# Kernel optimization log

Hardware: AMD Instinct MI355X
Metric: run time of the kernel (lower is better)

The kernel has to match this reference:

```python
import jax, jax.numpy as jnp
import numpy as np

EPS = 1e-5  # torch LayerNorm default

def _ln(x, g, b):
    m = jnp.mean(x, axis=-1, keepdims=True)
    v = jnp.mean((x - m) ** 2, axis=-1, keepdims=True)
    return (x - m) * jax.lax.rsqrt(v + EPS) * g + b

def setup_inputs() -> dict:
    key = jax.random.key(0)
    ks = jax.random.split(key, 12)
    N_sup = N_res = 768
    c_z = 128   # input_dim
    c = 128     # num_intermediate_channel
    c_out = 128 # output_dim
    s = 0.02
    d = {}
    d["act_s"] = jax.random.normal(ks[0], (N_sup, N_sup, c_z), jnp.float32)
    d["act_r"] = jax.random.normal(ks[1], (N_res, N_res, c_z), jnp.float32)
    d["mask_r"] = (jax.random.uniform(ks[2], (N_res, N_res)) > 0.1).astype(jnp.float32)
    # input LayerNorm params
    d["ln_in_g"] = jnp.ones((c_z,), jnp.float32)
    d["ln_in_b"] = jnp.zeros((c_z,), jnp.float32)
    # projections (stored as [in, out], y = x @ W + b)
    d["w_lp"] = (jax.random.normal(ks[3], (c_z, c)) * s).astype(jnp.float32)
    d["b_lp"] = jnp.zeros((c,), jnp.float32)
    d["w_rp"] = (jax.random.normal(ks[4], (c_z, c)) * s).astype(jnp.float32)
    d["b_rp"] = jnp.zeros((c,), jnp.float32)
    # gates (bias_init=1)
    d["w_lg"] = (jax.random.normal(ks[5], (c_z, c)) * s).astype(jnp.float32)
    d["b_lg"] = jnp.ones((c,), jnp.float32)
    d["w_rg"] = (jax.random.normal(ks[6], (c_z, c)) * s).astype(jnp.float32)
    d["b_rg"] = jnp.ones((c,), jnp.float32)
    # center LayerNorm
    d["ln_c_g"] = jnp.ones((c,), jnp.float32)
    d["ln_c_b"] = jnp.zeros((c,), jnp.float32)
    # output projection
    d["w_out"] = (jax.random.normal(ks[7], (c, c_out)) * s).astype(jnp.float32)
    d["b_out"] = jnp.zeros((c_out,), jnp.float32)
    return d

def reference(act_s, act_r, mask_r, ln_in_g, ln_in_b, w_lp, b_lp, w_rp, b_rp,
              w_lg, b_lg, w_rg, b_rg, ln_c_g, ln_c_b, w_out, b_out):
    m = mask_r[..., None]                                   # [N_res, N_res, 1]
    s = _ln(act_s, ln_in_g, ln_in_b)                        # [N_sup, N_sup, c_z]
    r = _ln(act_r, ln_in_g, ln_in_b)                        # [N_res, N_res, c_z]
    left = (s @ w_lp + b_lp) * jax.nn.sigmoid(s @ w_lg + b_lg)
    right = (m * (r @ w_rp + b_rp)) * jax.nn.sigmoid(r @ w_rg + b_rg)
    left_line = left.sum(axis=0)                            # [N_sup, c] (aggr_by_row)
    right_line = right.sum(axis=0)                          # [N_res, c]
    act = jnp.einsum('ik,jk->ijk', left_line, right_line)   # [N_sup, N_res, c]
    act = _ln(act, ln_c_g, ln_c_b)
    return act @ w_out + b_out                              # [N_sup, N_res, c_out]
```

## Files before the change

kernel.cpp:

```cpp
#include <hip/hip_runtime.h>
#include <math.h>

#define NRES 768
#define C    128
#define LNEPS 1e-5f
#define TA   16
#define ACH  48
#define MI   16
#define NIT  (NRES / MI)
#define XBUF (MI * 256)
#define LHALF (ACH * NIT)

typedef __attribute__((ext_vector_type(8))) short bf16x8;
typedef __attribute__((ext_vector_type(4))) float f32x4;

__device__ __forceinline__ uint32_t pack_hi(uint32_t u0, uint32_t u1) {
    return (u1 & 0xFFFF0000u) | (u0 >> 16);
}

__device__ __forceinline__ void split2t(float a, float b, uint32_t& hi, uint32_t& lo) {
    const uint32_t ua = __float_as_uint(a), ub = __float_as_uint(b);
    const float ra = a - __uint_as_float(ua & 0xFFFF0000u);
    const float rb = b - __uint_as_float(ub & 0xFFFF0000u);
    hi = pack_hi(ua, ub);
    lo = pack_hi(__float_as_uint(ra), __float_as_uint(rb));
}

__device__ __forceinline__ void stage_row3(const float4& x, int row, int t,
                                           char* hiB, char* loB, char* sqB) {
    const int byte = (row * 256 + 8 * (t & 31)) ^ ((row & 15) << 4);
    uint2 uh, ul, uq;
    split2t(x.x, x.y, uh.x, ul.x);
    split2t(x.z, x.w, uh.y, ul.y);
    uq.x = pack_hi(__float_as_uint(x.x * x.x), __float_as_uint(x.y * x.y));
    uq.y = pack_hi(__float_as_uint(x.z * x.z), __float_as_uint(x.w * x.w));
    *(uint2*)(hiB + byte) = uh;
    *(uint2*)(loB + byte) = ul;
    *(uint2*)(sqB + byte) = uq;
}

__device__ __forceinline__ uint32_t bf16rn(float f) {
    uint32_t u = __float_as_uint(f);
    return (u + 0x7FFFu + ((u >> 16) & 1u)) >> 16;
}

__global__ __launch_bounds__(256, 3) void line_all(
    const float* __restrict__ act_s, const float* __restrict__ act_r,
    const float* __restrict__ mask,
    const float* __restrict__ ln_g, const float* __restrict__ ln_b,
    const float* __restrict__ w_lp, const float* __restrict__ b_lp,
    const float* __restrict__ w_rp, const float* __restrict__ b_rp,
    const float* __restrict__ w_lg, const float* __restrict__ b_lg,
    const float* __restrict__ w_rg, const float* __restrict__ b_rg,
    float* __restrict__ part)
{
    __shared__ char  sHi[XBUF];
    __shared__ char  sLo[XBUF];
    __shared__ char  sSq[XBUF];
    __shared__ float sM[TA * MI];

    const int t = threadIdx.x;
    const int w = t >> 6;
    const int l = t & 63;
    const int right = (blockIdx.x >= LHALF);
    const int bid2  = blockIdx.x - right * LHALF;
    const int i0  = (bid2 % NIT) * MI;
    const int ach = bid2 / NIT;
    const int a0  = ach * TA;

    const float* act = right ? act_r : act_s;
    const float* wP  = right ? w_rp : w_lp;
    const float* bP  = right ? b_rp : b_lp;
    const float* wG  = right ? w_rg : w_lg;
    const float* bG  = right ? b_rg : b_lg;

    bf16x8 bfr[4][4];
    float  sQ[4], cB[4];
#pragma unroll
    for (int nt = 0; nt < 4; ++nt) {
        const float* wsrc = (nt < 2) ? wP : wG;
        const int n = w * 32 + (nt & 1) * 16 + (l & 15);
        float sacc = 0.f, tacc = 0.f;
#pragma unroll
        for (int kk = 0; kk < 4; ++kk) {
            bf16x8 f;
#pragma unroll
            for (int jj = 0; jj < 8; ++jj) {
                const int k = kk * 32 + (l >> 4) * 8 + jj;
                const float wv = wsrc[k * C + n];
                const uint32_t q = bf16rn(ln_g[k] * wv);
                f[jj] = (short)q;
                sacc += __uint_as_float(q << 16);
                tacc += ln_b[k] * wv;
            }
            bfr[nt][kk] = f;
        }
        sacc += __shfl_xor(sacc, 16); sacc += __shfl_xor(sacc, 32);
        tacc += __shfl_xor(tacc, 16); tacc += __shfl_xor(tacc, 32);
        sQ[nt] = sacc;
        cB[nt] = tacc + ((nt < 2) ? bP[n] : bG[n]);
    }

    bf16x8 onesf;
#pragma unroll
    for (int jj = 0; jj < 8; ++jj) onesf[jj] = (short)0x3F80;

    if (right) {
        sM[t] = mask[(size_t)(a0 + (t >> 4)) * NRES + i0 + (t & 15)];
    }

    float lacc[2][4];
#pragma unroll
    for (int ntp = 0; ntp < 2; ++ntp)
#pragma unroll
        for (int jr = 0; jr < 4; ++jr) lacc[ntp][jr] = 0.f;

    const float* srcbase = act + (size_t)a0 * (NRES * C) + (size_t)i0 * C;

    float4 xv[2], xn[2];
#pragma unroll
    for (int j = 0; j < 2; ++j)
        xv[j] = *(const float4*)(srcbase + 4 * (t + 256 * j));

    for (int al = 0; al < TA; ++al) {
        if (al + 1 < TA) {
            const float* srcn = srcbase + (size_t)(al + 1) * (NRES * C);
#pragma unroll
            for (int j = 0; j < 2; ++j)
                xn[j] = *(const float4*)(srcn + 4 * (t + 256 * j));
        }

#pragma unroll
        for (int j = 0; j < 2; ++j)
            stage_row3(xv[j], (t >> 5) + 8 * j, t, sHi, sLo, sSq);
        __syncthreads();

        const f32x4 zero = {0.f, 0.f, 0.f, 0.f};
        f32x4 acc[4], accS = zero, accS2 = zero;
#pragma unroll
        for (int nt = 0; nt < 4; ++nt) acc[nt] = zero;

#pragma unroll
        for (int kk = 0; kk < 4; ++kk) {
            const int row  = l & 15;
            const int byte = (row * 256 + (kk * 32 + (l >> 4) * 8) * 2) ^ ((row & 15) << 4);
            const bf16x8 ah  = *(const bf16x8*)(sHi + byte);
            const bf16x8 alo = *(const bf16x8*)(sLo + byte);
            const bf16x8 asq = *(const bf16x8*)(sSq + byte);
            acc[0] = __builtin_amdgcn_mfma_f32_16x16x32_bf16(ah,  bfr[0][kk], acc[0], 0, 0, 0);
            acc[0] = __builtin_amdgcn_mfma_f32_16x16x32_bf16(alo, bfr[0][kk], acc[0], 0, 0, 0);
            acc[1] = __builtin_amdgcn_mfma_f32_16x16x32_bf16(ah,  bfr[1][kk], acc[1], 0, 0, 0);
            acc[1] = __builtin_amdgcn_mfma_f32_16x16x32_bf16(alo, bfr[1][kk], acc[1], 0, 0, 0);
            acc[2] = __builtin_amdgcn_mfma_f32_16x16x32_bf16(ah,  bfr[2][kk], acc[2], 0, 0, 0);
            acc[3] = __builtin_amdgcn_mfma_f32_16x16x32_bf16(ah,  bfr[3][kk], acc[3], 0, 0, 0);
            accS   = __builtin_amdgcn_mfma_f32_16x16x32_bf16(ah,  onesf, accS,  0, 0, 0);
            accS2  = __builtin_amdgcn_mfma_f32_16x16x32_bf16(asq, onesf, accS2, 0, 0, 0);
        }

        float mk[4] = {1.f, 1.f, 1.f, 1.f};
        if (right) {
            const float4 m4 = *(const float4*)&sM[al * MI + (l >> 4) * 4];
            mk[0] = m4.x; mk[1] = m4.y; mk[2] = m4.z; mk[3] = m4.w;
        }
#pragma unroll
        for (int jr = 0; jr < 4; ++jr) {
            const float m_  = accS[jr] * (1.f / C);
            const float var = accS2[jr] * (1.f / C) - m_ * m_;
            const float inv = rsqrtf(var + LNEPS);
#pragma unroll
            for (int ntp = 0; ntp < 2; ++ntp) {
                const float P = (acc[ntp][jr]     - m_ * sQ[ntp])     * inv + cB[ntp];
                const float G = (acc[ntp + 2][jr] - m_ * sQ[ntp + 2]) * inv + cB[ntp + 2];
                const float sg = __builtin_amdgcn_rcpf(1.f + __expf(-G));
                lacc[ntp][jr] += P * sg * mk[jr];
            }
        }
        __syncthreads();

        xv[0] = xn[0]; xv[1] = xn[1];
    }

    float* dst = part + ((size_t)right * ACH + ach) * (NRES * C);
#pragma unroll
    for (int ntp = 0; ntp < 2; ++ntp)
#pragma unroll
        for (int jr = 0; jr < 4; ++jr)
            dst[(size_t)(i0 + (l >> 4) * 4 + jr) * C +
                w * 32 + ntp * 16 + (l & 15)] = lacc[ntp][jr];
}

__global__ __launch_bounds__(256) void reduce2(const float* __restrict__ part,
                                               float* __restrict__ left_line,
                                               float* __restrict__ right_line) {
    const int half = (blockIdx.x >= 384);
    const int idx  = (blockIdx.x - half * 384) * 256 + threadIdx.x;
    const float* p = part + (size_t)half * ACH * NRES * C;
    float s = 0.f;
#pragma unroll 8
    for (int q = 0; q < ACH; ++q) s += p[(size_t)q * (NRES * C) + idx];
    (half ? right_line : left_line)[idx] = s;
}

__global__ __launch_bounds__(256, 3) void out_mfma(
    const float* __restrict__ lline,
    const float* __restrict__ rline,
    const float* __restrict__ cg, const float* __restrict__ cb,
    const float* __restrict__ wO, const float* __restrict__ bO,
    float* __restrict__ out)
{
    __shared__ char sHi[64 * 256];
    __shared__ char sLo[64 * 256];
    __shared__ char sSq[64 * 256];

    const int t = threadIdx.x;
    const int w = t >> 6;
    const int l = t & 63;
    const int i = blockIdx.x;

    bf16x8 bfr[2][4];
    float  sQ[2], cB[2];
#pragma unroll
    for (int nt = 0; nt < 2; ++nt) {
        const int n = w * 32 + nt * 16 + (l & 15);
        float sacc = 0.f, tacc = 0.f;
#pragma unroll
        for (int kk = 0; kk < 4; ++kk) {
            bf16x8 f;
#pragma unroll
            for (int jj = 0; jj < 8; ++jj) {
                const int k = kk * 32 + (l >> 4) * 8 + jj;
                const float wv = wO[k * C + n];
                const uint32_t q = bf16rn(cg[k] * wv);
                f[jj] = (short)q;
                sacc += __uint_as_float(q << 16);
                tacc += cb[k] * wv;
            }
            bfr[nt][kk] = f;
        }
        sacc += __shfl_xor(sacc, 16); sacc += __shfl_xor(sacc, 32);
        tacc += __shfl_xor(tacc, 16); tacc += __shfl_xor(tacc, 32);
        sQ[nt] = sacc;
        cB[nt] = tacc + bO[n];
    }

    bf16x8 onesf;
#pragma unroll
    for (int jj = 0; jj < 8; ++jj) onesf[jj] = (short)0x3F80;

    const int c4 = 4 * (t & 31);
    const float4 l4 = *(const float4*)(lline + (size_t)i * C + c4);

    for (int jt = 0; jt < 12; ++jt) {
        const int j0 = jt * 64;
        const float* rsrc = rline + (size_t)j0 * C;

        float4 rv[8];
#pragma unroll
        for (int j = 0; j < 8; ++j)
            rv[j] = *(const float4*)(rsrc + 4 * (t + 256 * j));
#pragma unroll
        for (int j = 0; j < 8; ++j) {
            float4 p;
            p.x = l4.x * rv[j].x; p.y = l4.y * rv[j].y;
            p.z = l4.z * rv[j].z; p.w = l4.w * rv[j].w;
            stage_row3(p, (t >> 5) + 8 * j, t, sHi, sLo, sSq);
        }
        __syncthreads();

        const f32x4 zero = {0.f, 0.f, 0.f, 0.f};
#pragma unroll
        for (int mt = 0; mt < 4; ++mt) {
            f32x4 acc[2], accS = zero, accS2 = zero;
#pragma unroll
            for (int nt = 0; nt < 2; ++nt) acc[nt] = zero;
#pragma unroll
            for (int kk = 0; kk < 4; ++kk) {
                const int row  = mt * 16 + (l & 15);
                const int byte = (row * 256 + (kk * 32 + (l >> 4) * 8) * 2) ^ ((row & 15) << 4);
                const bf16x8 ah  = *(const bf16x8*)(sHi + byte);
                const bf16x8 alo = *(const bf16x8*)(sLo + byte);
                const bf16x8 asq = *(const bf16x8*)(sSq + byte);
                acc[0] = __builtin_amdgcn_mfma_f32_16x16x32_bf16(ah,  bfr[0][kk], acc[0], 0, 0, 0);
                acc[0] = __builtin_amdgcn_mfma_f32_16x16x32_bf16(alo, bfr[0][kk], acc[0], 0, 0, 0);
                acc[1] = __builtin_amdgcn_mfma_f32_16x16x32_bf16(ah,  bfr[1][kk], acc[1], 0, 0, 0);
                acc[1] = __builtin_amdgcn_mfma_f32_16x16x32_bf16(alo, bfr[1][kk], acc[1], 0, 0, 0);
                accS  = __builtin_amdgcn_mfma_f32_16x16x32_bf16(ah,  onesf, accS,  0, 0, 0);
                accS2 = __builtin_amdgcn_mfma_f32_16x16x32_bf16(asq, onesf, accS2, 0, 0, 0);
            }
#pragma unroll
            for (int jr = 0; jr < 4; ++jr) {
                const float m_  = accS[jr] * (1.f / C);
                const float var = accS2[jr] * (1.f / C) - m_ * m_;
                const float inv = rsqrtf(var + LNEPS);
#pragma unroll
                for (int nt = 0; nt < 2; ++nt)
                    out[((size_t)i * NRES + j0 + mt * 16 + (l >> 4) * 4 + jr) * C +
                        w * 32 + nt * 16 + (l & 15)] =
                        (acc[nt][jr] - m_ * sQ[nt]) * inv + cB[nt];
            }
        }
        __syncthreads();
    }
}

extern "C" void kernel_launch(void* const* d_in, const int* in_sizes, int n_in,
                              void* d_out, int out_size, void* d_ws, size_t ws_size,
                              hipStream_t stream) {
    const float* act_s = (const float*)d_in[0];
    const float* act_r = (const float*)d_in[1];
    const float* mask  = (const float*)d_in[2];
    const float* ln_g  = (const float*)d_in[3];
    const float* ln_b  = (const float*)d_in[4];
    const float* w_lp  = (const float*)d_in[5];
    const float* b_lp  = (const float*)d_in[6];
    const float* w_rp  = (const float*)d_in[7];
    const float* b_rp  = (const float*)d_in[8];
    const float* w_lg  = (const float*)d_in[9];
    const float* b_lg  = (const float*)d_in[10];
    const float* w_rg  = (const float*)d_in[11];
    const float* b_rg  = (const float*)d_in[12];
    const float* ln_cg = (const float*)d_in[13];
    const float* ln_cb = (const float*)d_in[14];
    const float* w_out = (const float*)d_in[15];
    const float* b_out = (const float*)d_in[16];
    float* out = (float*)d_out;

    float* part       = (float*)d_ws;
    float* left_line  = part + (size_t)2 * ACH * NRES * C;
    float* right_line = left_line + NRES * C;

    line_all<<<2 * LHALF, 256, 0, stream>>>(act_s, act_r, mask, ln_g, ln_b,
                                            w_lp, b_lp, w_rp, b_rp,
                                            w_lg, b_lg, w_rg, b_rg, part);
    reduce2<<<768, 256, 0, stream>>>(part, left_line, right_line);
    out_mfma<<<NRES, 256, 0, stream>>>(left_line, right_line, ln_cg, ln_cb,
                                       w_out, b_out, out);
}
```

Measured before the change: 337.3 us.

## Replace split-bf16 hi/lo MFMA with single fp16 MFMA and scaled activations

Both kernels drop the bf16 hi/lo split (two MFMAs per projection tile plus a third LDS buffer) and instead stage a single fp16 copy of the activations and their squares. This removes the low-part LDS buffer, its stores and loads, and two MFMAs per k-step. In the output kernel the outer product is pre-scaled by 1/64 to keep squared values within fp16 range, and epsilon is rescaled to compensate. The risk is lower precision and possible overflow or underflow for inputs outside the expected range.

```diff
diff --git a/kernel.cpp b/kernel.cpp
--- a/kernel.cpp
+++ b/kernel.cpp
@@ -10,38 +10,28 @@
 #define NIT  (NRES / MI)
 #define XBUF (MI * 256)
 #define LHALF (ACH * NIT)
-
-typedef __attribute__((ext_vector_type(8))) short bf16x8;
-typedef __attribute__((ext_vector_type(4))) float f32x4;
-
-__device__ __forceinline__ uint32_t pack_hi(uint32_t u0, uint32_t u1) {
-    return (u1 & 0xFFFF0000u) | (u0 >> 16);
-}
-
-__device__ __forceinline__ void split2t(float a, float b, uint32_t& hi, uint32_t& lo) {
-    const uint32_t ua = __float_as_uint(a), ub = __float_as_uint(b);
-    const float ra = a - __uint_as_float(ua & 0xFFFF0000u);
-    const float rb = b - __uint_as_float(ub & 0xFFFF0000u);
-    hi = pack_hi(ua, ub);
-    lo = pack_hi(__float_as_uint(ra), __float_as_uint(rb));
-}
-
-__device__ __forceinline__ void stage_row3(const float4& x, int row, int t,
-                                           char* hiB, char* loB, char* sqB) {
+#define OSC  0.015625f
+
+typedef __attribute__((ext_vector_type(8))) _Float16 f16x8;
+typedef __attribute__((ext_vector_type(4))) float   f32x4;
+
+__device__ __forceinline__ uint32_t pk_f16rn(float a, float b) {
+    _Float16 ha = (_Float16)a, hb = (_Float16)b;
+    const uint32_t ua = *(const unsigned short*)&ha;
+    const uint32_t ub = *(const unsigned short*)&hb;
+    return ua | (ub << 16);
+}
+
+__device__ __forceinline__ void stage_row2(const float4& x, int row, int t,
+                                           char* hiB, char* sqB) {
     const int byte = (row * 256 + 8 * (t & 31)) ^ ((row & 15) << 4);
-    uint2 uh, ul, uq;
-    split2t(x.x, x.y, uh.x, ul.x);
-    split2t(x.z, x.w, uh.y, ul.y);
-    uq.x = pack_hi(__float_as_uint(x.x * x.x), __float_as_uint(x.y * x.y));
-    uq.y = pack_hi(__float_as_uint(x.z * x.z), __float_as_uint(x.w * x.w));
+    uint2 uh, uq;
+    uh.x = pk_f16rn(x.x, x.y);
+    uh.y = pk_f16rn(x.z, x.w);
+    uq.x = pk_f16rn(x.x * x.x, x.y * x.y);
+    uq.y = pk_f16rn(x.z * x.z, x.w * x.w);
     *(uint2*)(hiB + byte) = uh;
-    *(uint2*)(loB + byte) = ul;
     *(uint2*)(sqB + byte) = uq;
-}
-
-__device__ __forceinline__ uint32_t bf16rn(float f) {
-    uint32_t u = __float_as_uint(f);
-    return (u + 0x7FFFu + ((u >> 16) & 1u)) >> 16;
 }
 
 __global__ __launch_bounds__(256, 3) void line_all(
@@ -55,7 +45,6 @@
     float* __restrict__ part)
 {
     __shared__ char  sHi[XBUF];
-    __shared__ char  sLo[XBUF];
     __shared__ char  sSq[XBUF];
     __shared__ float sM[TA * MI];
 
@@ -74,8 +63,8 @@
     const float* wG  = right ? w_rg : w_lg;
     const float* bG  = right ? b_rg : b_lg;
 
-    bf16x8 bfr[4][4];
-    float  sQ[4], cB[4];
+    f16x8 bfr[4][4];
+    float sQ[4], cB[4];
 #pragma unroll
     for (int nt = 0; nt < 4; ++nt) {
         const float* wsrc = (nt < 2) ? wP : wG;
@@ -83,14 +72,14 @@
         float sacc = 0.f, tacc = 0.f;
 #pragma unroll
         for (int kk = 0; kk < 4; ++kk) {
-            bf16x8 f;
+            f16x8 f;
 #pragma unroll
             for (int jj = 0; jj < 8; ++jj) {
                 const int k = kk * 32 + (l >> 4) * 8 + jj;
                 const float wv = wsrc[k * C + n];
-                const uint32_t q = bf16rn(ln_g[k] * wv);
-                f[jj] = (short)q;
-                sacc += __uint_as_float(q << 16);
+                const _Float16 q = (_Float16)(ln_g[k] * wv);
+                f[jj] = q;
+                sacc += (float)q;
                 tacc += ln_b[k] * wv;
             }
             bfr[nt][kk] = f;
@@ -101,9 +90,9 @@
         cB[nt] = tacc + ((nt < 2) ? bP[n] : bG[n]);
     }
 
-    bf16x8 onesf;
-#pragma unroll
-    for (int jj = 0; jj < 8; ++jj) onesf[jj] = (short)0x3F80;
+    f16x8 onesf;
+#pragma unroll
+    for (int jj = 0; jj < 8; ++jj) onesf[jj] = (_Float16)1.0f;
 
     if (right) {
         sM[t] = mask[(size_t)(a0 + (t >> 4)) * NRES + i0 + (t & 15)];
@@ -132,7 +121,7 @@
 
 #pragma unroll
         for (int j = 0; j < 2; ++j)
-            stage_row3(xv[j], (t >> 5) + 8 * j, t, sHi, sLo, sSq);
+            stage_row2(xv[j], (t >> 5) + 8 * j, t, sHi, sSq);
         __syncthreads();
 
         const f32x4 zero = {0.f, 0.f, 0.f, 0.f};
@@ -144,17 +133,14 @@
         for (int kk = 0; kk < 4; ++kk) {
             const int row  = l & 15;
             const int byte = (row * 256 + (kk * 32 + (l >> 4) * 8) * 2) ^ ((row & 15) << 4);
-            const bf16x8 ah  = *(const bf16x8*)(sHi + byte);
-            const bf16x8 alo = *(const bf16x8*)(sLo + byte);
-            const bf16x8 asq = *(const bf16x8*)(sSq + byte);
-            acc[0] = __builtin_amdgcn_mfma_f32_16x16x32_bf16(ah,  bfr[0][kk], acc[0], 0, 0, 0);
-            acc[0] = __builtin_amdgcn_mfma_f32_16x16x32_bf16(alo, bfr[0][kk], acc[0], 0, 0, 0);
-            acc[1] = __builtin_amdgcn_mfma_f32_16x16x32_bf16(ah,  bfr[1][kk], acc[1], 0, 0, 0);
-            acc[1] = __builtin_amdgcn_mfma_f32_16x16x32_bf16(alo, bfr[1][kk], acc[1], 0, 0, 0);
-            acc[2] = __builtin_amdgcn_mfma_f32_16x16x32_bf16(ah,  bfr[2][kk], acc[2], 0, 0, 0);
-            acc[3] = __builtin_amdgcn_mfma_f32_16x16x32_bf16(ah,  bfr[3][kk], acc[3], 0, 0, 0);
-            accS   = __builtin_amdgcn_mfma_f32_16x16x32_bf16(ah,  onesf, accS,  0, 0, 0);
-            accS2  = __builtin_amdgcn_mfma_f32_16x16x32_bf16(asq, onesf, accS2, 0, 0, 0);
+            const f16x8 ah  = *(const f16x8*)(sHi + byte);
+            const f16x8 asq = *(const f16x8*)(sSq + byte);
+            acc[0] = __builtin_amdgcn_mfma_f32_16x16x32_f16(ah,  bfr[0][kk], acc[0], 0, 0, 0);
+            acc[1] = __builtin_amdgcn_mfma_f32_16x16x32_f16(ah,  bfr[1][kk], acc[1], 0, 0, 0);
+            acc[2] = __builtin_amdgcn_mfma_f32_16x16x32_f16(ah,  bfr[2][kk], acc[2], 0, 0, 0);
+            acc[3] = __builtin_amdgcn_mfma_f32_16x16x32_f16(ah,  bfr[3][kk], acc[3], 0, 0, 0);
+            accS   = __builtin_amdgcn_mfma_f32_16x16x32_f16(ah,  onesf, accS,  0, 0, 0);
+            accS2  = __builtin_amdgcn_mfma_f32_16x16x32_f16(asq, onesf, accS2, 0, 0, 0);
         }
 
         float mk[4] = {1.f, 1.f, 1.f, 1.f};
@@ -209,7 +195,6 @@
     float* __restrict__ out)
 {
     __shared__ char sHi[64 * 256];
-    __shared__ char sLo[64 * 256];
     __shared__ char sSq[64 * 256];
 
     const int t = threadIdx.x;
@@ -217,22 +202,22 @@
     const int l = t & 63;
     const int i = blockIdx.x;
 
-    bf16x8 bfr[2][4];
-    float  sQ[2], cB[2];
+    f16x8 bfr[2][4];
+    float sQ[2], cB[2];
 #pragma unroll
     for (int nt = 0; nt < 2; ++nt) {
         const int n = w * 32 + nt * 16 + (l & 15);
         float sacc = 0.f, tacc = 0.f;
 #pragma unroll
         for (int kk = 0; kk < 4; ++kk) {
-            bf16x8 f;
+            f16x8 f;
 #pragma unroll
             for (int jj = 0; jj < 8; ++jj) {
                 const int k = kk * 32 + (l >> 4) * 8 + jj;
                 const float wv = wO[k * C + n];
-                const uint32_t q = bf16rn(cg[k] * wv);
-                f[jj] = (short)q;
-                sacc += __uint_as_float(q << 16);
+                const _Float16 q = (_Float16)(cg[k] * wv);
+                f[jj] = q;
+                sacc += (float)q;
                 tacc += cb[k] * wv;
             }
             bfr[nt][kk] = f;
@@ -243,12 +228,13 @@
         cB[nt] = tacc + bO[n];
     }
 
-    bf16x8 onesf;
-#pragma unroll
-    for (int jj = 0; jj < 8; ++jj) onesf[jj] = (short)0x3F80;
+    f16x8 onesf;
+#pragma unroll
+    for (int jj = 0; jj < 8; ++jj) onesf[jj] = (_Float16)1.0f;
 
     const int c4 = 4 * (t & 31);
-    const float4 l4 = *(const float4*)(lline + (size_t)i * C + c4);
+    float4 l4 = *(const float4*)(lline + (size_t)i * C + c4);
+    l4.x *= OSC; l4.y *= OSC; l4.z *= OSC; l4.w *= OSC;
 
     for (int jt = 0; jt < 12; ++jt) {
         const int j0 = jt * 64;
@@ -263,7 +249,7 @@
             float4 p;
             p.x = l4.x * rv[j].x; p.y = l4.y * rv[j].y;
             p.z = l4.z * rv[j].z; p.w = l4.w * rv[j].w;
-            stage_row3(p, (t >> 5) + 8 * j, t, sHi, sLo, sSq);
+            stage_row2(p, (t >> 5) + 8 * j, t, sHi, sSq);
         }
         __syncthreads();
 
@@ -277,21 +263,18 @@
             for (int kk = 0; kk < 4; ++kk) {
                 const int row  = mt * 16 + (l & 15);
                 const int byte = (row * 256 + (kk * 32 + (l >> 4) * 8) * 2) ^ ((row & 15) << 4);
-                const bf16x8 ah  = *(const bf16x8*)(sHi + byte);
-                const bf16x8 alo = *(const bf16x8*)(sLo + byte);
-                const bf16x8 asq = *(const bf16x8*)(sSq + byte);
-                acc[0] = __builtin_amdgcn_mfma_f32_16x16x32_bf16(ah,  bfr[0][kk], acc[0], 0, 0, 0);
-                acc[0] = __builtin_amdgcn_mfma_f32_16x16x32_bf16(alo, bfr[0][kk], acc[0], 0, 0, 0);
-                acc[1] = __builtin_amdgcn_mfma_f32_16x16x32_bf16(ah,  bfr[1][kk], acc[1], 0, 0, 0);
-                acc[1] = __builtin_amdgcn_mfma_f32_16x16x32_bf16(alo, bfr[1][kk], acc[1], 0, 0, 0);
-                accS  = __builtin_amdgcn_mfma_f32_16x16x32_bf16(ah,  onesf, accS,  0, 0, 0);
-                accS2 = __builtin_amdgcn_mfma_f32_16x16x32_bf16(asq, onesf, accS2, 0, 0, 0);
+                const f16x8 ah  = *(const f16x8*)(sHi + byte);
+                const f16x8 asq = *(const f16x8*)(sSq + byte);
+                acc[0] = __builtin_amdgcn_mfma_f32_16x16x32_f16(ah,  bfr[0][kk], acc[0], 0, 0, 0);
+                acc[1] = __builtin_amdgcn_mfma_f32_16x16x32_f16(ah,  bfr[1][kk], acc[1], 0, 0, 0);
+                accS   = __builtin_amdgcn_mfma_f32_16x16x32_f16(ah,  onesf, accS,  0, 0, 0);
+                accS2  = __builtin_amdgcn_mfma_f32_16x16x32_f16(asq, onesf, accS2, 0, 0, 0);
             }
 #pragma unroll
             for (int jr = 0; jr < 4; ++jr) {
                 const float m_  = accS[jr] * (1.f / C);
                 const float var = accS2[jr] * (1.f / C) - m_ * m_;
-                const float inv = rsqrtf(var + LNEPS);
+                const float inv = rsqrtf(var + LNEPS * OSC * OSC);
 #pragma unroll
                 for (int nt = 0; nt < 2; ++nt)
                     out[((size_t)i * NRES + j0 + mt * 16 + (l >> 4) * 4 + jr) * C +
```

New measurement: 360.3 us. 6.8% more time.
